# Kernel tuning notes

Measured on AMD Instinct MI355X. Metric: run time of the kernel, lower is better.

The kernel has to match this reference:

```python
import jax, jax.numpy as jnp
import numpy as np


def pconv(x, W, b):
    # 1x1x1 Conv3d == pointwise linear over channels. x: [B,Ci,T,H,W], W: [Co,Ci], b: [Co]
    return jnp.einsum('bcthw,oc->bothw', x, W) + b[None, :, None, None, None]


def setup_inputs() -> dict:
    key = jax.random.key(0)
    ks = jax.random.split(key, 12)
    B, C, T, H, W = 2, 512, 16, 16, 16
    ni, nc = 6, 10

    def w(k, co, ci):
        return (jax.random.normal(k, (co, ci), jnp.float32) / np.sqrt(ci)).astype(jnp.float32)

    return {
        'features': jax.random.normal(ks[0], (B, C, T, H, W), jnp.float32),
        'cam': jax.random.uniform(ks[1], (B, ni, T, H, W), jnp.float32),
        'Wc': w(ks[2], ni, C),  'bc': jnp.zeros((ni,), jnp.float32),
        'Wq': w(ks[3], ni, ni), 'bq': jnp.zeros((ni,), jnp.float32),
        'Wk': w(ks[4], ni, ni), 'bk': jnp.zeros((ni,), jnp.float32),
        'Wv': w(ks[5], ni, ni), 'bv': jnp.zeros((ni,), jnp.float32),
        'Wcq': w(ks[6], ni, ni), 'bcq': jnp.zeros((ni,), jnp.float32),
        'Wck': w(ks[7], ni, ni), 'bck': jnp.zeros((ni,), jnp.float32),
        'Wo': w(ks[8], nc, ni), 'bo': jnp.zeros((nc,), jnp.float32),
        'beta': jnp.zeros((1,), jnp.float32),
    }


def reference(features, cam, Wc, bc, Wq, bq, Wk, bk, Wv, bv, Wcq, bcq, Wck, bck, Wo, bo, beta):
    B, _, T, H, W = features.shape
    ni = Wq.shape[0]
    N = T * H * W

    context = jax.nn.relu(pconv(features, Wc, bc))          # [B,ni,T,H,W]
    Q = pconv(context, Wq, bq)
    K = pconv(context, Wk, bk)
    V = pconv(context, Wv, bv)

    # cam is already at size (T,H,W): trilinear resize to the same size is identity
    cam_resized = cam
    QD = pconv(cam_resized, Wcq, bcq)
    KD = pconv(cam_resized, Wck, bck)

    qf = Q.reshape(B, ni, N)
    kf = K.reshape(B, ni, N)
    vf = V.reshape(B, ni, N)
    qdf = QD.reshape(B, ni, N)
    kdf = KD.reshape(B, ni, N)

    # dual low-rank NxN score matrices (d = ni = 6)
    P_nd = jnp.einsum('bdn,bdm->bnm', qf, kf)               # [B,N,N]
    P_d = jnp.einsum('bdn,bdm->bnm', qdf, kdf)              # [B,N,N]
    scale = jnp.asarray(np.sqrt(ni), jnp.float32)
    attention = jax.nn.softmax(P_d * P_nd / scale, axis=-1)  # [B,N,N]

    enhancement = jnp.einsum('bnm,bdm->bdn', attention, vf).reshape(B, ni, T, H, W)
    enhanced = context + beta[0] * enhancement

    output_maps = pconv(enhanced, Wo, bo)                   # [B,nc,T,H,W]
    logits = output_maps.mean(axis=(2, 3, 4))               # [B,nc]
    return output_maps, logits
```

## Files before the change

kernel.cpp:

```cpp
#include <hip/hip_runtime.h>
#include <math.h>

#define NI 6
#define NC 10
#define C_IN 512
#define N_POS 4096
#define B_SZ 2


__global__ __launch_bounds__(512) void k_fused(
    const float* __restrict__ feat, const float* __restrict__ cam,
    const float* __restrict__ Wc,  const float* __restrict__ bc,
    const float* __restrict__ Wq,  const float* __restrict__ bq,
    const float* __restrict__ Wk,  const float* __restrict__ bk,
    const float* __restrict__ Wv,  const float* __restrict__ bv,
    const float* __restrict__ Wcq, const float* __restrict__ bcq,
    const float* __restrict__ Wck, const float* __restrict__ bck,
    const float* __restrict__ Wo,  const float* __restrict__ bo,
    const float* __restrict__ beta,
    float* __restrict__ ctx, float* __restrict__ qb, float* __restrict__ kb,
    float* __restrict__ vb, float* __restrict__ qdb, float* __restrict__ kdb,
    float* __restrict__ partial, float* __restrict__ out, int* __restrict__ counter)
{
    __shared__ float sW[C_IN * 8];
    __shared__ float sPart[64 * 8 * 25];
    __shared__ float sE[32 * NI];

    const int t   = threadIdx.x;
    const int bid = blockIdx.x;
    const int b   = bid >> 7;
    const int n0  = (bid & 127) * 32;

    if (bid == 0 && t == 0) *counter = 0;

    const int q  = t & 7;
    const int ch = t >> 3;
    const float* f = feat + (size_t)b * C_IN * N_POS + n0 + q * 4;

    float wreg[6];
    #pragma unroll
    for (int i0 = 0; i0 < 6; ++i0) wreg[i0] = Wc[t + i0 * 512];

    float4 x[8];
    #pragma unroll
    for (int cc = 0; cc < 8; ++cc)
        x[cc] = *(const float4*)(f + (size_t)(cc * 64 + ch) * N_POS);

    #pragma unroll
    for (int i0 = 0; i0 < 6; ++i0) {
        const int i = t + i0 * 512;
        sW[(i & 511) * 8 + (i >> 9)] = wreg[i0];
    }
    __syncthreads();

    float acc[24];
    #pragma unroll
    for (int i = 0; i < 24; ++i) acc[i] = 0.f;

    #pragma unroll
    for (int cc = 0; cc < 8; ++cc) {
        const int c = cc * 64 + ch;
        const float4 xx = x[cc];
        const float4 w0 = *(const float4*)(&sW[c * 8]);
        const float2 w1 = *(const float2*)(&sW[c * 8 + 4]);
        acc[0]  += w0.x * xx.x; acc[6]  += w0.x * xx.y; acc[12] += w0.x * xx.z; acc[18] += w0.x * xx.w;
        acc[1]  += w0.y * xx.x; acc[7]  += w0.y * xx.y; acc[13] += w0.y * xx.z; acc[19] += w0.y * xx.w;
        acc[2]  += w0.z * xx.x; acc[8]  += w0.z * xx.y; acc[14] += w0.z * xx.z; acc[20] += w0.z * xx.w;
        acc[3]  += w0.w * xx.x; acc[9]  += w0.w * xx.y; acc[15] += w0.w * xx.z; acc[21] += w0.w * xx.w;
        acc[4]  += w1.x * xx.x; acc[10] += w1.x * xx.y; acc[16] += w1.x * xx.z; acc[22] += w1.x * xx.w;
        acc[5]  += w1.y * xx.x; acc[11] += w1.y * xx.y; acc[17] += w1.y * xx.z; acc[23] += w1.y * xx.w;
    }

    {
        float* sp = &sPart[t * 25];
        #pragma unroll
        for (int j = 0; j < 24; ++j) sp[j] = acc[j];
    }
    __syncthreads();

    const float bt = *beta;

    if (t < 192) {
        const int pos = t / 6, d = t - pos * 6;
        const int qq = pos >> 2, po = pos & 3;
        float s = bc[d];
        #pragma unroll
        for (int c2 = 0; c2 < 64; ++c2)
            s += sPart[(c2 * 8 + qq) * 25 + po * 6 + d];
        const float ov = fmaxf(s, 0.f);
        if (bt != 0.f) ctx[(size_t)bid * 192 + t] = ov;
        sE[t] = ov;
    }
    __syncthreads();

    {
        const int ps = t & 31, o = t >> 5;
        if (o < NC) {
            float s = 0.f;
            #pragma unroll
            for (int d = 0; d < NI; ++d) s += Wo[o * NI + d] * sE[ps * NI + d];
            out[((size_t)(b * NC + o)) * N_POS + n0 + ps] = s + bo[o];
            #pragma unroll
            for (int off = 16; off > 0; off >>= 1) s += __shfl_down(s, off, 32);
            if (ps == 0) partial[o * 256 + bid] = s;
        }
    }

    if (bt != 0.f && t < 32) {
        const int p = bid * 32 + t;
        const int n = n0 + t;
        float e[NI], cv[NI];
        #pragma unroll
        for (int d = 0; d < NI; ++d) e[d] = sE[t * NI + d];
        #pragma unroll
        for (int d = 0; d < NI; ++d)
            cv[d] = cam[((size_t)(b * NI + d)) * N_POS + n];
        #pragma unroll
        for (int o = 0; o < NI; ++o) {
            float s1 = bq[o], s2 = bk[o], s3 = bv[o], s4 = bcq[o], s5 = bck[o];
            #pragma unroll
            for (int d = 0; d < NI; ++d) {
                s1 += Wq[o * NI + d] * e[d];
                s2 += Wk[o * NI + d] * e[d];
                s3 += Wv[o * NI + d] * e[d];
                s4 += Wcq[o * NI + d] * cv[d];
                s5 += Wck[o * NI + d] * cv[d];
            }
            qb[(size_t)p * NI + o]  = s1;
            kb[(size_t)p * NI + o]  = s2;
            vb[(size_t)p * NI + o]  = s3;
            qdb[(size_t)p * NI + o] = s4;
            kdb[(size_t)p * NI + o] = s5;
        }
    }
}

__global__ __launch_bounds__(256) void k_attn(
    const float* __restrict__ beta,
    const float* __restrict__ q,  const float* __restrict__ k,
    const float* __restrict__ v,  const float* __restrict__ qd,
    const float* __restrict__ kd, const float* __restrict__ ctx,
    const float* __restrict__ Wo, const float* __restrict__ bo,
    float* __restrict__ out, float* __restrict__ partial,
    int* __restrict__ counter, float* __restrict__ logits)
{
    const float bt = *beta;
    const int t = threadIdx.x;

    if (bt == 0.f) {
        if (blockIdx.x == 0 && t < 160) {
            const int combo = t >> 3, lane8 = t & 7;
            const int b = combo / NC, o = combo - b * NC;
            float s = 0.f;
            #pragma unroll
            for (int j = 0; j < 16; ++j)
                s += partial[o * 256 + b * 128 + lane8 * 16 + j];
            #pragma unroll
            for (int off = 4; off > 0; off >>= 1) s += __shfl_down(s, off, 8);
            if (lane8 == 0) logits[b * NC + o] = s * (1.f / 4096.f) + bo[o];
        }
        return;
    }

    __shared__ float sO[64][NC];
    __shared__ int lastFlag;

    {
        const float inv_scale = 0.40824829046386296f;
        const int r = t >> 2, lane4 = t & 3;
        const int p = blockIdx.x * 64 + r;
        const int b = p >> 12, n = p & 4095;
        const int base = b << 12;

        float qr[NI], qdr[NI];
        {
            const float* qp  = q  + (size_t)p * NI;
            const float* qdp = qd + (size_t)p * NI;
            #pragma unroll
            for (int d = 0; d < NI; ++d) { qr[d] = qp[d]; qdr[d] = qdp[d]; }
        }

        float mmax = -INFINITY, l = 0.f;
        float acc[NI] = {0.f, 0.f, 0.f, 0.f, 0.f, 0.f};

        for (int mi = 0; mi < 1024; ++mi) {
            const int m = mi * 4 + lane4;
            const float* kp  = k  + (size_t)(base + m) * NI;
            const float* kdp = kd + (size_t)(base + m) * NI;
            const float* vp  = v  + (size_t)(base + m) * NI;
            float s1 = 0.f, s2 = 0.f;
            #pragma unroll
            for (int d = 0; d < NI; ++d) { s1 += qr[d] * kp[d]; s2 += qdr[d] * kdp[d]; }
            const float s = s1 * s2 * inv_scale;
            const float nm = fmaxf(mmax, s);
            const float corr = __expf(mmax - nm);
            const float e = __expf(s - nm);
            l = l * corr + e;
            #pragma unroll
            for (int d = 0; d < NI; ++d) acc[d] = acc[d] * corr + e * vp[d];
            mmax = nm;
        }

        #pragma unroll
        for (int off = 1; off < 4; off <<= 1) {
            const float om = __shfl_xor(mmax, off);
            const float ol = __shfl_xor(l, off);
            const float nm = fmaxf(mmax, om);
            const float c1 = __expf(mmax - nm);
            const float c2 = __expf(om - nm);
            l = l * c1 + ol * c2;
            #pragma unroll
            for (int d = 0; d < NI; ++d)
                acc[d] = acc[d] * c1 + __shfl_xor(acc[d], off) * c2;
            mmax = nm;
        }

        if (lane4 == 0) {
            const float invl = 1.f / l;
            float e[NI];
            const float* cp = ctx + (size_t)p * NI;
            #pragma unroll
            for (int d = 0; d < NI; ++d) e[d] = cp[d] + bt * acc[d] * invl;
            #pragma unroll
            for (int o = 0; o < NC; ++o) {
                float s = 0.f;
                #pragma unroll
                for (int d = 0; d < NI; ++d) s += Wo[o * NI + d] * e[d];
                out[((size_t)(b * NC + o)) * N_POS + n] = s + bo[o];
                sO[r][o] = s;
            }
        }
        __syncthreads();

        if (t < 2 * NC) {
            const int half = t / NC, o = t - half * NC;
            float s = 0.f;
            #pragma unroll
            for (int rr = 0; rr < 32; ++rr) s += sO[half * 32 + rr][o];
            partial[o * 256 + blockIdx.x * 2 + half] = s;
        }
    }

    __threadfence();
    __syncthreads();
    if (t == 0) lastFlag = (atomicAdd(counter, 1) == 127);
    __syncthreads();
    if (lastFlag) {
        __threadfence();
        if (t < 160) {
            const int combo = t >> 3, lane8 = t & 7;
            const int b = combo / NC, o = combo - b * NC;
            float s = 0.f;
            #pragma unroll
            for (int j = 0; j < 16; ++j)
                s += partial[o * 256 + b * 128 + lane8 * 16 + j];
            #pragma unroll
            for (int off = 4; off > 0; off >>= 1) s += __shfl_down(s, off, 8);
            if (lane8 == 0) logits[b * NC + o] = s * (1.f / 4096.f) + bo[o];
        }
    }
}

extern "C" void kernel_launch(void* const* d_in, const int* in_sizes, int n_in,
                              void* d_out, int out_size, void* d_ws, size_t ws_size,
                              hipStream_t stream)
{
    const float* feat = (const float*)d_in[0];
    const float* cam  = (const float*)d_in[1];
    const float* Wc  = (const float*)d_in[2];  const float* bc  = (const float*)d_in[3];
    const float* Wq  = (const float*)d_in[4];  const float* bq  = (const float*)d_in[5];
    const float* Wk  = (const float*)d_in[6];  const float* bk  = (const float*)d_in[7];
    const float* Wv  = (const float*)d_in[8];  const float* bv  = (const float*)d_in[9];
    const float* Wcq = (const float*)d_in[10]; const float* bcq = (const float*)d_in[11];
    const float* Wck = (const float*)d_in[12]; const float* bck = (const float*)d_in[13];
    const float* Wo  = (const float*)d_in[14]; const float* bo  = (const float*)d_in[15];
    const float* beta = (const float*)d_in[16];

    float* ws = (float*)d_ws;
    float* ctx     = ws;
    float* qb      = ws + 49152;
    float* kb      = ws + 98304;
    float* vb      = ws + 147456;
    float* qdb     = ws + 196608;
    float* kdb     = ws + 245760;
    float* partial = ws + 294912;
    int*   counter = (int*)(ws + 297472);

    float* out    = (float*)d_out;
    float* logits = out + (size_t)B_SZ * NC * N_POS;

    k_fused<<<256, 512, 0, stream>>>(feat, cam, Wc, bc, Wq, bq, Wk, bk, Wv, bv,
                                     Wcq, bcq, Wck, bck, Wo, bo, beta,
                                     ctx, qb, kb, vb, qdb, kdb, partial, out, counter);
    k_attn<<<128, 256, 0, stream>>>(beta, qb, kb, vb, qdb, kdb, ctx, Wo, bo,
                                    out, partial, counter, logits);
}
```

Baseline: 11.27 us.

## Replace multi-block attention tail with single-block kernel, dropping atomic counter

```diff
diff --git a/kernel.cpp b/kernel.cpp
--- a/kernel.cpp
+++ b/kernel.cpp
@@ -20,7 +20,7 @@
     const float* __restrict__ beta,
     float* __restrict__ ctx, float* __restrict__ qb, float* __restrict__ kb,
     float* __restrict__ vb, float* __restrict__ qdb, float* __restrict__ kdb,
-    float* __restrict__ partial, float* __restrict__ out, int* __restrict__ counter)
+    float* __restrict__ partial, float* __restrict__ out)
 {
     __shared__ float sW[C_IN * 8];
     __shared__ float sPart[64 * 8 * 25];
@@ -30,8 +30,6 @@
     const int bid = blockIdx.x;
     const int b   = bid >> 7;
     const int n0  = (bid & 127) * 32;
-
-    if (bid == 0 && t == 0) *counter = 0;
 
     const int q  = t & 7;
     const int ch = t >> 3;
@@ -135,20 +133,20 @@
     }
 }
 
-__global__ __launch_bounds__(256) void k_attn(
+__global__ __launch_bounds__(256) void k_tail(
     const float* __restrict__ beta,
     const float* __restrict__ q,  const float* __restrict__ k,
     const float* __restrict__ v,  const float* __restrict__ qd,
     const float* __restrict__ kd, const float* __restrict__ ctx,
     const float* __restrict__ Wo, const float* __restrict__ bo,
-    float* __restrict__ out, float* __restrict__ partial,
-    int* __restrict__ counter, float* __restrict__ logits)
+    float* __restrict__ out, const float* __restrict__ partial,
+    float* __restrict__ logits)
 {
     const float bt = *beta;
     const int t = threadIdx.x;
 
     if (bt == 0.f) {
-        if (blockIdx.x == 0 && t < 160) {
+        if (t < 160) {
             const int combo = t >> 3, lane8 = t & 7;
             const int b = combo / NC, o = combo - b * NC;
             float s = 0.f;
@@ -162,13 +160,19 @@
         return;
     }
 
-    __shared__ float sO[64][NC];
-    __shared__ int lastFlag;
-
-    {
-        const float inv_scale = 0.40824829046386296f;
-        const int r = t >> 2, lane4 = t & 3;
-        const int p = blockIdx.x * 64 + r;
+    __shared__ float sRed[64][2 * NC];
+
+    const float inv_scale = 0.40824829046386296f;
+    const int rt = t >> 2, lane4 = t & 3;
+
+    float lacc[2][NC];
+    #pragma unroll
+    for (int bb = 0; bb < 2; ++bb)
+        #pragma unroll
+        for (int o = 0; o < NC; ++o) lacc[bb][o] = 0.f;
+
+    for (int rr0 = 0; rr0 < B_SZ * N_POS; rr0 += 64) {
+        const int p = rr0 + rt;
         const int b = p >> 12, n = p & 4095;
         const int base = b << 12;
 
@@ -185,12 +189,13 @@
 
         for (int mi = 0; mi < 1024; ++mi) {
             const int m = mi * 4 + lane4;
-            const float* kp  = k  + (size_t)(base + m) * NI;
+            const float* kp  = kd - 0 + (size_t)0;
+            const float* kpp = k  + (size_t)(base + m) * NI;
             const float* kdp = kd + (size_t)(base + m) * NI;
             const float* vp  = v  + (size_t)(base + m) * NI;
             float s1 = 0.f, s2 = 0.f;
             #pragma unroll
-            for (int d = 0; d < NI; ++d) { s1 += qr[d] * kp[d]; s2 += qdr[d] * kdp[d]; }
+            for (int d = 0; d < NI; ++d) { s1 += qr[d] * kpp[d]; s2 += qdr[d] * kdp[d]; }
             const float s = s1 * s2 * inv_scale;
             const float nm = fmaxf(mmax, s);
             const float corr = __expf(mmax - nm);
@@ -199,6 +204,7 @@
             #pragma unroll
             for (int d = 0; d < NI; ++d) acc[d] = acc[d] * corr + e * vp[d];
             mmax = nm;
+            (void)kp;
         }
 
         #pragma unroll
@@ -227,37 +233,24 @@
                 #pragma unroll
                 for (int d = 0; d < NI; ++d) s += Wo[o * NI + d] * e[d];
                 out[((size_t)(b * NC + o)) * N_POS + n] = s + bo[o];
-                sO[r][o] = s;
+                lacc[b][o] += s;
             }
         }
-        __syncthreads();
-
-        if (t < 2 * NC) {
-            const int half = t / NC, o = t - half * NC;
-            float s = 0.f;
-            #pragma unroll
-            for (int rr = 0; rr < 32; ++rr) s += sO[half * 32 + rr][o];
-            partial[o * 256 + blockIdx.x * 2 + half] = s;
-        }
-    }
-
-    __threadfence();
-    __syncthreads();
-    if (t == 0) lastFlag = (atomicAdd(counter, 1) == 127);
-    __syncthreads();
-    if (lastFlag) {
-        __threadfence();
-        if (t < 160) {
-            const int combo = t >> 3, lane8 = t & 7;
-            const int b = combo / NC, o = combo - b * NC;
-            float s = 0.f;
-            #pragma unroll
-            for (int j = 0; j < 16; ++j)
-                s += partial[o * 256 + b * 128 + lane8 * 16 + j];
-            #pragma unroll
-            for (int off = 4; off > 0; off >>= 1) s += __shfl_down(s, off, 8);
-            if (lane8 == 0) logits[b * NC + o] = s * (1.f / 4096.f) + bo[o];
-        }
+    }
+
+    if (lane4 == 0) {
+        #pragma unroll
+        for (int bb = 0; bb < 2; ++bb)
+            #pragma unroll
+            for (int o = 0; o < NC; ++o) sRed[rt][bb * NC + o] = lacc[bb][o];
+    }
+    __syncthreads();
+    if (t < 2 * NC) {
+        const int bb = t / NC, o = t - bb * NC;
+        float s = 0.f;
+        #pragma unroll
+        for (int r = 0; r < 64; ++r) s += sRed[r][bb * NC + o];
+        logits[bb * NC + o] = s * (1.f / 4096.f) + bo[o];
     }
 }
 
@@ -284,14 +277,13 @@
     float* qdb     = ws + 196608;
     float* kdb     = ws + 245760;
     float* partial = ws + 294912;
-    int*   counter = (int*)(ws + 297472);
 
     float* out    = (float*)d_out;
     float* logits = out + (size_t)B_SZ * NC * N_POS;
 
     k_fused<<<256, 512, 0, stream>>>(feat, cam, Wc, bc, Wq, bq, Wk, bk, Wv, bv,
                                      Wcq, bcq, Wck, bck, Wo, bo, beta,
-                                     ctx, qb, kb, vb, qdb, kdb, partial, out, counter);
-    k_attn<<<128, 256, 0, stream>>>(beta, qb, kb, vb, qdb, kdb, ctx, Wo, bo,
-                                    out, partial, counter, logits);
+                                     ctx, qb, kb, vb, qdb, kdb, partial, out);
+    k_tail<<<1, 256, 0, stream>>>(beta, qb, kb, vb, qdb, kdb, ctx, Wo, bo,
+                                  out, partial, logits);
 }
```

Measured after the change: 13.29 us. 1.18x slower.
